# Kernel optimization log

Measured on AMD Instinct MI355X. Metric: run time of the kernel, lower is better.

## Reference

```python
import jax, jax.numpy as jnp
import numpy as np

NUM_HEADS = 32
NUM_KV_HEADS = 8
HEAD_SIZE = 128
SCALE = 0.08838834764831845  # 1/sqrt(128)
BATCH = 32
MAX_BLOCKS_PER_SEQ = 128
BLOCK_SIZE = 16
NUM_BLOCKS = BATCH * MAX_BLOCKS_PER_SEQ  # 4096
MAX_CTX = MAX_BLOCKS_PER_SEQ * BLOCK_SIZE  # 2048


def setup_inputs() -> dict:
    key = jax.random.key(0)
    ks = jax.random.split(key, 8)
    query = jax.random.normal(ks[0], (BATCH, 1, NUM_HEADS * HEAD_SIZE), dtype=jnp.float32)
    k_new = jax.random.normal(ks[1], (BATCH, 1, NUM_KV_HEADS * HEAD_SIZE), dtype=jnp.float32)
    v_new = jax.random.normal(ks[2], (BATCH, 1, NUM_KV_HEADS * HEAD_SIZE), dtype=jnp.float32)
    key_cache = jax.random.normal(ks[3], (NUM_BLOCKS, NUM_KV_HEADS, HEAD_SIZE, BLOCK_SIZE), dtype=jnp.float32)
    value_cache = jax.random.normal(ks[4], (NUM_BLOCKS, NUM_KV_HEADS, HEAD_SIZE, BLOCK_SIZE), dtype=jnp.float32)
    # each sequence owns a contiguous stripe of blocks, accessed through the table
    block_tables = jnp.arange(NUM_BLOCKS, dtype=jnp.int32).reshape(BATCH, MAX_BLOCKS_PER_SEQ)
    context_lens = jax.random.randint(ks[5], (BATCH,), 1, MAX_CTX + 1, dtype=jnp.int32)
    # slot for the newly-decoded token (position context_len-1)
    last = context_lens - 1
    blk_idx = block_tables[jnp.arange(BATCH), last // BLOCK_SIZE]
    slot_mapping = (blk_idx * BLOCK_SIZE + last % BLOCK_SIZE).reshape(BATCH, 1).astype(jnp.int32)
    return {
        "query": query, "key": k_new, "value": v_new,
        "key_cache": key_cache, "value_cache": value_cache,
        "block_tables": block_tables, "context_lens": context_lens,
        "slot_mapping": slot_mapping,
    }


def reference(query, key, value, key_cache, value_cache, block_tables, context_lens, slot_mapping):
    B = query.shape[0]
    block_size = value_cache.shape[3]
    q_per_kv = NUM_HEADS // NUM_KV_HEADS

    # --- reshape_and_cache: write new k/v into paged caches at slot_mapping ---
    slots = slot_mapping.reshape(-1)                       # [B] (seq_len=1 decode)
    blk = slots // block_size
    off = slots % block_size
    k_new = key.reshape(B, NUM_KV_HEADS, HEAD_SIZE)
    v_new = value.reshape(B, NUM_KV_HEADS, HEAD_SIZE)
    key_cache = key_cache.at[blk, :, :, off].set(k_new)
    value_cache = value_cache.at[blk, :, :, off].set(v_new)

    # --- paged_attention_v1: gather blocks via block_tables, masked softmax ---
    # [B, MB, KVH, D, bs] -> [B, MB, bs, KVH, D] -> [B, T, KVH, D]
    K = jnp.moveaxis(key_cache[block_tables], -1, 2).reshape(B, -1, NUM_KV_HEADS, HEAD_SIZE)
    V = jnp.moveaxis(value_cache[block_tables], -1, 2).reshape(B, -1, NUM_KV_HEADS, HEAD_SIZE)
    T = K.shape[1]

    q = query.reshape(B, NUM_KV_HEADS, q_per_kv, HEAD_SIZE)
    scores = jnp.einsum('bkqd,btkd->bkqt', q, K) * SCALE   # [B, KVH, Qper, T]
    valid = (jnp.arange(T, dtype=jnp.int32)[None, :] < context_lens[:, None])
    scores = jnp.where(valid[:, None, None, :], scores, jnp.finfo(scores.dtype).min)
    probs = jax.nn.softmax(scores, axis=-1)
    out = jnp.einsum('bkqt,btkd->bkqd', probs, V)          # [B, KVH, Qper, D]
    return out.reshape(B, 1, NUM_HEADS * HEAD_SIZE)
```

## Files before the change

### kernel.cpp

```cpp
#include <hip/hip_runtime.h>
#include <float.h>

#define NUM_HEADS    32
#define NUM_KV_HEADS 8
#define HEAD_SIZE    128
#define Q_PER_KV     4
#define BLOCK_SZ     16
#define MAX_BLOCKS   128
#define SCALE        0.08838834764831845f

#define CHUNK_BLOCKS 16
#define CHUNK_TOK    (CHUNK_BLOCKS * BLOCK_SZ)
#define NCHUNK       (MAX_BLOCKS / CHUNK_BLOCKS)
#define WS_STRIDE    528

typedef float v4f __attribute__((ext_vector_type(4)));

__global__ __launch_bounds__(64, 4)
void paged_attn_chunk(const float* __restrict__ query,
                      const float* __restrict__ key_cache,
                      const float* __restrict__ value_cache,
                      const int* __restrict__ block_tables,
                      const int* __restrict__ context_lens,
                      float* __restrict__ ws) {
    const int c   = blockIdx.x;
    const int h   = blockIdx.y;
    const int b   = blockIdx.z;
    const int tid = threadIdx.x;

    const int ctx = context_lens[b];
    const int nb  = (ctx + BLOCK_SZ - 1) / BLOCK_SZ;
    const int b0  = c * CHUNK_BLOCKS;
    if (b0 >= nb) return;
    const int nbl  = min(nb - b0, CHUNK_BLOCKS);
    const int last = ctx - 1;

    __shared__ float q_lds[Q_PER_KV * HEAD_SIZE];
    __shared__ float s_lds[Q_PER_KV * CHUNK_TOK];

    {
        const v4f* qg = reinterpret_cast<const v4f*>(
            query + ((size_t)b * NUM_HEADS + h * Q_PER_KV) * HEAD_SIZE);
        v4f* ql = reinterpret_cast<v4f*>(q_lds);
        ql[tid]      = qg[tid]      * SCALE;
        ql[tid + 64] = qg[tid + 64] * SCALE;
    }
    __syncthreads();

    {
        const int bil = tid >> 2;
        const int o   = tid & 3;
        if (bil < nbl) {
            const int phys = block_tables[b * MAX_BLOCKS + b0 + bil];
            const v4f* kp = reinterpret_cast<const v4f*>(key_cache) +
                            ((size_t)phys * NUM_KV_HEADS + h) * (HEAD_SIZE * BLOCK_SZ / 4);
            const v4f* q4 = reinterpret_cast<const v4f*>(q_lds);
            v4f acc[Q_PER_KV];
            #pragma unroll
            for (int qh = 0; qh < Q_PER_KV; ++qh) acc[qh] = (v4f)0.f;
            #pragma unroll 4
            for (int d4 = 0; d4 < HEAD_SIZE / 4; ++d4) {
                v4f k[4];
                #pragma unroll
                for (int dd = 0; dd < 4; ++dd) k[dd] = kp[d4 * 16 + dd * 4 + o];
                #pragma unroll
                for (int qh = 0; qh < Q_PER_KV; ++qh) {
                    const v4f qv = q4[qh * (HEAD_SIZE / 4) + d4];
                    #pragma unroll
                    for (int dd = 0; dd < 4; ++dd) acc[qh] += qv[dd] * k[dd];
                }
            }
            const int t0 = bil * BLOCK_SZ + o * 4;
            const int g0 = b0 * BLOCK_SZ + t0;
            #pragma unroll
            for (int qh = 0; qh < Q_PER_KV; ++qh) {
                v4f sv;
                #pragma unroll
                for (int j = 0; j < 4; ++j) {
                    const int g = g0 + j;
                    sv[j] = (g < ctx && g != last) ? acc[qh][j] : -FLT_MAX;
                }
                *reinterpret_cast<v4f*>(&s_lds[qh * CHUNK_TOK + t0]) = sv;
            }
        }
    }
    __syncthreads();

    float* wsp = ws + (((size_t)b * NUM_KV_HEADS + h) * NCHUNK + c) * WS_STRIDE;
    {
        const int T = nbl * BLOCK_SZ;
        #pragma unroll
        for (int qh = 0; qh < Q_PER_KV; ++qh) {
            float m = -FLT_MAX;
            for (int t = tid; t < T; t += 64) m = fmaxf(m, s_lds[qh * CHUNK_TOK + t]);
            #pragma unroll
            for (int off = 32; off; off >>= 1) m = fmaxf(m, __shfl_xor(m, off));
            float l = 0.f;
            for (int t = tid; t < T; t += 64) {
                const float s = s_lds[qh * CHUNK_TOK + t];
                const float p = (s == -FLT_MAX) ? 0.f : __expf(s - m);
                s_lds[qh * CHUNK_TOK + t] = p;
                l += p;
            }
            #pragma unroll
            for (int off = 32; off; off >>= 1) l += __shfl_xor(l, off);
            if (tid == 0) { wsp[qh] = m; wsp[Q_PER_KV + qh] = l; }
        }
    }
    __syncthreads();

    {
        const int d0 = tid, d1 = tid + 64;
        float acc0[Q_PER_KV] = {0.f, 0.f, 0.f, 0.f};
        float acc1[Q_PER_KV] = {0.f, 0.f, 0.f, 0.f};
        for (int bil = 0; bil < nbl; ++bil) {
            const int phys = block_tables[b * MAX_BLOCKS + b0 + bil];
            const v4f* vp = reinterpret_cast<const v4f*>(value_cache) +
                            ((size_t)phys * NUM_KV_HEADS + h) * (HEAD_SIZE * BLOCK_SZ / 4);
            v4f vv0[4], vv1[4];
            #pragma unroll
            for (int j = 0; j < 4; ++j) { vv0[j] = vp[d0 * 4 + j]; vv1[j] = vp[d1 * 4 + j]; }
            #pragma unroll
            for (int qh = 0; qh < Q_PER_KV; ++qh) {
                const v4f* pq = reinterpret_cast<const v4f*>(
                    &s_lds[qh * CHUNK_TOK + bil * BLOCK_SZ]);
                #pragma unroll
                for (int j = 0; j < 4; ++j) {
                    const v4f p = pq[j];
                    acc0[qh] += p[0]*vv0[j][0] + p[1]*vv0[j][1] + p[2]*vv0[j][2] + p[3]*vv0[j][3];
                    acc1[qh] += p[0]*vv1[j][0] + p[1]*vv1[j][1] + p[2]*vv1[j][2] + p[3]*vv1[j][3];
                }
            }
        }
        float* wo = wsp + 2 * Q_PER_KV;
        #pragma unroll
        for (int qh = 0; qh < Q_PER_KV; ++qh) {
            wo[qh * HEAD_SIZE + d0] = acc0[qh];
            wo[qh * HEAD_SIZE + d1] = acc1[qh];
        }
    }
}

__global__ __launch_bounds__(512, 2)
void paged_attn_reduce(const float* __restrict__ query,
                       const float* __restrict__ k_new,
                       const float* __restrict__ v_new,
                       const int* __restrict__ context_lens,
                       const float* __restrict__ ws,
                       float* __restrict__ out) {
    const int h   = blockIdx.x;
    const int b   = blockIdx.y;
    const int tid = threadIdx.x;

    __shared__ float snew_lds[Q_PER_KV];

    const int ctx = context_lens[b];
    const int nb  = (ctx + BLOCK_SZ - 1) / BLOCK_SZ;
    const int nch = (nb + CHUNK_BLOCKS - 1) / CHUNK_BLOCKS;

    if (tid < 4 * 64) {
        const int w = tid >> 6, lane = tid & 63;
        const float* qp = query + ((size_t)b * NUM_HEADS + h * Q_PER_KV + w) * HEAD_SIZE;
        const float* kn = k_new + ((size_t)b * NUM_KV_HEADS + h) * HEAD_SIZE;
        float v = qp[lane] * kn[lane] + qp[lane + 64] * kn[lane + 64];
        #pragma unroll
        for (int off = 32; off; off >>= 1) v += __shfl_xor(v, off);
        if (lane == 0) snew_lds[w] = v * SCALE;
    }
    __syncthreads();

    const int qh = tid >> 7, d = tid & 127;
    const float* wsb = ws + ((size_t)b * NUM_KV_HEADS + h) * NCHUNK * WS_STRIDE;

    float M = -FLT_MAX, L = 0.f, acc = 0.f;
    for (int c = 0; c < nch; ++c) {
        const float* wsp = wsb + (size_t)c * WS_STRIDE;
        const float mc = wsp[qh];
        const float lc = wsp[Q_PER_KV + qh];
        const float oc = wsp[2 * Q_PER_KV + qh * HEAD_SIZE + d];
        const float nM = fmaxf(M, mc);
        const float eM = __expf(M - nM), ec = __expf(mc - nM);
        acc = acc * eM + oc * ec;
        L   = L   * eM + lc * ec;
        M   = nM;
    }
    {
        const float s  = snew_lds[qh];
        const float nM = fmaxf(M, s);
        const float eM = __expf(M - nM), es = __expf(s - nM);
        const float vn = v_new[((size_t)b * NUM_KV_HEADS + h) * HEAD_SIZE + d];
        acc = acc * eM + es * vn;
        L   = L   * eM + es;
    }
    out[((size_t)b * NUM_HEADS + h * Q_PER_KV + qh) * HEAD_SIZE + d] = acc / L;
}

extern "C" void kernel_launch(void* const* d_in, const int* in_sizes, int n_in,
                              void* d_out, int out_size, void* d_ws, size_t ws_size,
                              hipStream_t stream) {
    const float* query       = (const float*)d_in[0];
    const float* k_new       = (const float*)d_in[1];
    const float* v_new       = (const float*)d_in[2];
    const float* key_cache   = (const float*)d_in[3];
    const float* value_cache = (const float*)d_in[4];
    const int*   block_tables  = (const int*)d_in[5];
    const int*   context_lens  = (const int*)d_in[6];
    float* out = (float*)d_out;
    float* ws  = (float*)d_ws;

    const int batch = in_sizes[6];

    dim3 g1(NCHUNK, NUM_KV_HEADS, batch);
    paged_attn_chunk<<<g1, 64, 0, stream>>>(query, key_cache, value_cache,
                                            block_tables, context_lens, ws);
    dim3 g2(NUM_KV_HEADS, batch);
    paged_attn_reduce<<<g2, 512, 0, stream>>>(query, k_new, v_new,
                                              context_lens, ws, out);
}
```

Measured before the change: 79.52 us.

## Prefetch V blocks with double buffering and reorder grid so chunk index is outermost

```diff
diff --git a/kernel.cpp b/kernel.cpp
--- a/kernel.cpp
+++ b/kernel.cpp
@@ -23,9 +23,9 @@
                       const int* __restrict__ block_tables,
                       const int* __restrict__ context_lens,
                       float* __restrict__ ws) {
-    const int c   = blockIdx.x;
-    const int h   = blockIdx.y;
-    const int b   = blockIdx.z;
+    const int h   = blockIdx.x;
+    const int b   = blockIdx.y;
+    const int c   = blockIdx.z;
     const int tid = threadIdx.x;
 
     const int ctx = context_lens[b];
@@ -86,6 +86,23 @@
     }
     __syncthreads();
 
+    const int d0 = tid, d1 = tid + 64;
+    v4f A0[4], A1[4], B0[4], B1[4];
+    {
+        const int phys0 = block_tables[b * MAX_BLOCKS + b0];
+        const v4f* vp0 = reinterpret_cast<const v4f*>(value_cache) +
+                         ((size_t)phys0 * NUM_KV_HEADS + h) * (HEAD_SIZE * BLOCK_SZ / 4);
+        #pragma unroll
+        for (int j = 0; j < 4; ++j) { A0[j] = vp0[d0 * 4 + j]; A1[j] = vp0[d1 * 4 + j]; }
+        if (nbl > 1) {
+            const int phys1 = block_tables[b * MAX_BLOCKS + b0 + 1];
+            const v4f* vp1 = reinterpret_cast<const v4f*>(value_cache) +
+                             ((size_t)phys1 * NUM_KV_HEADS + h) * (HEAD_SIZE * BLOCK_SZ / 4);
+            #pragma unroll
+            for (int j = 0; j < 4; ++j) { B0[j] = vp1[d0 * 4 + j]; B1[j] = vp1[d1 * 4 + j]; }
+        }
+    }
+
     float* wsp = ws + (((size_t)b * NUM_KV_HEADS + h) * NCHUNK + c) * WS_STRIDE;
     {
         const int T = nbl * BLOCK_SZ;
@@ -110,16 +127,10 @@
     __syncthreads();
 
     {
-        const int d0 = tid, d1 = tid + 64;
         float acc0[Q_PER_KV] = {0.f, 0.f, 0.f, 0.f};
         float acc1[Q_PER_KV] = {0.f, 0.f, 0.f, 0.f};
-        for (int bil = 0; bil < nbl; ++bil) {
-            const int phys = block_tables[b * MAX_BLOCKS + b0 + bil];
-            const v4f* vp = reinterpret_cast<const v4f*>(value_cache) +
-                            ((size_t)phys * NUM_KV_HEADS + h) * (HEAD_SIZE * BLOCK_SZ / 4);
-            v4f vv0[4], vv1[4];
-            #pragma unroll
-            for (int j = 0; j < 4; ++j) { vv0[j] = vp[d0 * 4 + j]; vv1[j] = vp[d1 * 4 + j]; }
+
+        for (int bil = 0; bil < nbl; bil += 2) {
             #pragma unroll
             for (int qh = 0; qh < Q_PER_KV; ++qh) {
                 const v4f* pq = reinterpret_cast<const v4f*>(
@@ -127,11 +138,39 @@
                 #pragma unroll
                 for (int j = 0; j < 4; ++j) {
                     const v4f p = pq[j];
-                    acc0[qh] += p[0]*vv0[j][0] + p[1]*vv0[j][1] + p[2]*vv0[j][2] + p[3]*vv0[j][3];
-                    acc1[qh] += p[0]*vv1[j][0] + p[1]*vv1[j][1] + p[2]*vv1[j][2] + p[3]*vv1[j][3];
-                }
-            }
-        }
+                    acc0[qh] += p[0]*A0[j][0] + p[1]*A0[j][1] + p[2]*A0[j][2] + p[3]*A0[j][3];
+                    acc1[qh] += p[0]*A1[j][0] + p[1]*A1[j][1] + p[2]*A1[j][2] + p[3]*A1[j][3];
+                }
+            }
+            if (bil + 2 < nbl) {
+                const int phys = block_tables[b * MAX_BLOCKS + b0 + bil + 2];
+                const v4f* vp = reinterpret_cast<const v4f*>(value_cache) +
+                                ((size_t)phys * NUM_KV_HEADS + h) * (HEAD_SIZE * BLOCK_SZ / 4);
+                #pragma unroll
+                for (int j = 0; j < 4; ++j) { A0[j] = vp[d0 * 4 + j]; A1[j] = vp[d1 * 4 + j]; }
+            }
+            if (bil + 1 < nbl) {
+                #pragma unroll
+                for (int qh = 0; qh < Q_PER_KV; ++qh) {
+                    const v4f* pq = reinterpret_cast<const v4f*>(
+                        &s_lds[qh * CHUNK_TOK + (bil + 1) * BLOCK_SZ]);
+                    #pragma unroll
+                    for (int j = 0; j < 4; ++j) {
+                        const v4f p = pq[j];
+                        acc0[qh] += p[0]*B0[j][0] + p[1]*B0[j][1] + p[2]*B0[j][2] + p[3]*B0[j][3];
+                        acc1[qh] += p[0]*B1[j][0] + p[1]*B1[j][1] + p[2]*B1[j][2] + p[3]*B1[j][3];
+                    }
+                }
+                if (bil + 3 < nbl) {
+                    const int phys = block_tables[b * MAX_BLOCKS + b0 + bil + 3];
+                    const v4f* vp = reinterpret_cast<const v4f*>(value_cache) +
+                                    ((size_t)phys * NUM_KV_HEADS + h) * (HEAD_SIZE * BLOCK_SZ / 4);
+                    #pragma unroll
+                    for (int j = 0; j < 4; ++j) { B0[j] = vp[d0 * 4 + j]; B1[j] = vp[d1 * 4 + j]; }
+                }
+            }
+        }
+
         float* wo = wsp + 2 * Q_PER_KV;
         #pragma unroll
         for (int qh = 0; qh < Q_PER_KV; ++qh) {
@@ -210,7 +249,7 @@
 
     const int batch = in_sizes[6];
 
-    dim3 g1(NCHUNK, NUM_KV_HEADS, batch);
+    dim3 g1(NUM_KV_HEADS, batch, NCHUNK);
     paged_attn_chunk<<<g1, 64, 0, stream>>>(query, key_cache, value_cache,
                                             block_tables, context_lens, ws);
     dim3 g2(NUM_KV_HEADS, batch);
```

Measured after the change: 138.9 us. +74.7%, slower.
